# Kernel optimization log

Hardware: AMD Instinct MI355X
Metric: run time of the kernel (lower is better)

Reference implementation:

```python
import jax, jax.numpy as jnp
import numpy as np

B, LS, VS = 4, 1024, 1024
VH, LH, H = 1024, 1024, 16
HD = LH // H  # head_dim = 64


def setup_inputs() -> dict:
    key = jax.random.key(0)
    ks = jax.random.split(key, 10)
    s = 0.02
    return {
        "v_hidden_states": jax.random.normal(ks[0], (B, VS, VH), jnp.float32),
        "l_hidden_states": jax.random.normal(ks[1], (B, LS, LH), jnp.float32),
        "q_w": jax.random.normal(ks[2], (LH, LH), jnp.float32) * s,
        "q_b": jnp.zeros((LH,), jnp.float32),
        "k_w": jax.random.normal(ks[3], (VH, LH), jnp.float32) * s,
        "k_b": jnp.zeros((LH,), jnp.float32),
        "v_w": jax.random.normal(ks[4], (VH, LH), jnp.float32) * s,
        "v_b": jnp.zeros((LH,), jnp.float32),
        "o_w": jax.random.normal(ks[5], (LH, LH), jnp.float32) * s,
        "o_b": jnp.zeros((LH,), jnp.float32),
    }


def reference(v_hidden_states, l_hidden_states, q_w, q_b, k_w, k_b, v_w, v_b, o_w, o_b):
    b, ls, _ = l_hidden_states.shape
    vs = v_hidden_states.shape[1]
    q = (l_hidden_states @ q_w + q_b).reshape(b, ls, H, HD)
    k = (v_hidden_states @ k_w + k_b).reshape(b, vs, H, HD)
    v = (v_hidden_states @ v_w + v_b).reshape(b, vs, H, HD)
    # NOTE: original scales by sqrt(hidden_size), not sqrt(head_dim)
    scale = jnp.sqrt(jnp.asarray(LH, q.dtype))
    scores = jnp.einsum("blhd,bvhd->bhlv", q, k) / scale
    attn = jax.nn.softmax(scores, axis=-1)
    out = jnp.einsum("bhlv,bvhd->blhd", attn, v).reshape(b, ls, LH)
    return out @ o_w + o_b
```

## Files before the change

kernel.cpp:

```cpp
#include <hip/hip_runtime.h>

typedef __bf16 bf16;
typedef __attribute__((ext_vector_type(4))) __bf16 bf16x4;
typedef __attribute__((ext_vector_type(8))) __bf16 bf16x8;
typedef __attribute__((ext_vector_type(4))) float f32x4;

static __device__ __forceinline__ f32x4 mfma_16x16x32(bf16x8 a, bf16x8 b, f32x4 c) {
    return __builtin_amdgcn_mfma_f32_16x16x32_bf16(a, b, c, 0, 0, 0);
}

static __device__ __forceinline__ bf16x8 load8(const float* p) {
    f32x4 a = *(const f32x4*)p;
    f32x4 b = *(const f32x4*)(p + 4);
    bf16x8 r;
    r[0] = (bf16)a[0]; r[1] = (bf16)a[1]; r[2] = (bf16)a[2]; r[3] = (bf16)a[3];
    r[4] = (bf16)b[0]; r[5] = (bf16)b[1]; r[6] = (bf16)b[2]; r[7] = (bf16)b[3];
    return r;
}

static __device__ __forceinline__ void gload_lds16(const void* g, void* l) {
    __builtin_amdgcn_global_load_lds(
        (const __attribute__((address_space(1))) void*)g,
        (__attribute__((address_space(3))) void*)l, 16, 0, 0);
}

__global__ __launch_bounds__(256) void prep_kernel(
    const float* __restrict__ l_h, const float* __restrict__ v_h,
    const float* __restrict__ w0, const float* __restrict__ w1,
    const float* __restrict__ w2, const float* __restrict__ w3,
    bf16* __restrict__ l_bf, bf16* __restrict__ v_bf,
    bf16* __restrict__ dq, bf16* __restrict__ dkv, bf16* __restrict__ dov)
{
    const int id = blockIdx.x;
    if (id < 4096) {
        const float* s = (id < 2048) ? l_h : v_h;
        bf16*       d = (id < 2048) ? l_bf : v_bf;
        const int   bb = (id < 2048) ? id : id - 2048;
        const size_t i = ((size_t)bb * 256 + threadIdx.x) * 8;
        *(bf16x8*)(d + i) = load8(s + i);
        return;
    }
    const int widx = id - 4096;
    const int z    = widx >> 8;
    const int rem  = widx & 255;
    const int j0   = (rem & 15) * 64;
    const int i0   = (rem >> 4) * 64;
    const float* src; bf16* dst;
    switch (z) {
        case 0:  src = w0; dst = dq; break;
        case 1:  src = w1; dst = dkv; break;
        case 2:  src = w2; dst = dkv + (size_t)1024 * 1024; break;
        default: src = w3; dst = dov; break;
    }
    __shared__ float T[64][65];
    const int tx = threadIdx.x & 15;
    const int ty = threadIdx.x >> 4;
    #pragma unroll
    for (int it = 0; it < 4; ++it) {
        f32x4 v = *(const f32x4*)(src + (size_t)(i0 + ty + it * 16) * 1024 + j0 + tx * 4);
        T[ty + it * 16][tx * 4 + 0] = v[0];
        T[ty + it * 16][tx * 4 + 1] = v[1];
        T[ty + it * 16][tx * 4 + 2] = v[2];
        T[ty + it * 16][tx * 4 + 3] = v[3];
    }
    __syncthreads();
    #pragma unroll
    for (int it = 0; it < 4; ++it) {
        const int jj = ty + it * 16;
        bf16x4 o;
        o[0] = (bf16)T[tx * 4 + 0][jj];
        o[1] = (bf16)T[tx * 4 + 1][jj];
        o[2] = (bf16)T[tx * 4 + 2][jj];
        o[3] = (bf16)T[tx * 4 + 3][jj];
        *(bf16x4*)(dst + (size_t)(j0 + jj) * 1024 + i0 + tx * 4) = o;
    }
}

__global__ __launch_bounds__(256, 2) void proj128_kernel(
    const bf16* __restrict__ l_bf, const bf16* __restrict__ v_bf,
    const bf16* __restrict__ QWt,  const bf16* __restrict__ KVWt,
    const float* __restrict__ q_b, const float* __restrict__ k_b,
    const float* __restrict__ v_b,
    bf16* __restrict__ Qh, bf16* __restrict__ Kh, bf16* __restrict__ Vt)
{
    __shared__ __align__(16) bf16 As[128][32];
    __shared__ __align__(16) bf16 Bs[128][32];

    const int t    = threadIdx.x;
    const int lane = t & 63;
    const int wave = t >> 6;
    const int wm   = wave & 1;
    const int wn   = wave >> 1;
    const int l15  = lane & 15;
    const int quad = lane >> 4;

    const bool isQ = blockIdx.x < 8;
    const bf16* A  = isQ ? l_bf : v_bf;
    const bf16* Bt = isQ ? QWt  : KVWt;
    const int  gn0 = (isQ ? blockIdx.x : blockIdx.x - 8) * 128;
    const int  gm0 = blockIdx.y * 128;
    const int  K   = 1024;

    const int srow    = lane >> 2;
    const int chunk_g = (lane & 3) ^ ((srow >> 1) & 3);
    const size_t aoff = (size_t)(gm0 + wave * 32 + srow) * K + chunk_g * 8;
    const size_t boff = (size_t)(gn0 + wave * 32 + srow) * K + chunk_g * 8;

    f32x4 acc[4][4];
    #pragma unroll
    for (int i = 0; i < 4; ++i)
        #pragma unroll
        for (int j = 0; j < 4; ++j)
            acc[i][j] = (f32x4){0.f, 0.f, 0.f, 0.f};

    for (int k0 = 0; k0 < K; k0 += 32) {
        #pragma unroll
        for (int q = 0; q < 2; ++q) {
            gload_lds16(A  + aoff + (size_t)q * 16 * K + k0, &As[wave * 32 + q * 16][0]);
            gload_lds16(Bt + boff + (size_t)q * 16 * K + k0, &Bs[wave * 32 + q * 16][0]);
        }
        __syncthreads();

        bf16x8 af[4], bfr[4];
        #pragma unroll
        for (int mt = 0; mt < 4; ++mt) {
            const int row = wm * 64 + mt * 16 + l15;
            af[mt] = *(const bf16x8*)(&As[row][(quad ^ ((row >> 1) & 3)) * 8]);
        }
        #pragma unroll
        for (int nt = 0; nt < 4; ++nt) {
            const int row = wn * 64 + nt * 16 + l15;
            bfr[nt] = *(const bf16x8*)(&Bs[row][(quad ^ ((row >> 1) & 3)) * 8]);
        }
        #pragma unroll
        for (int mt = 0; mt < 4; ++mt)
            #pragma unroll
            for (int nt = 0; nt < 4; ++nt)
                acc[mt][nt] = mfma_16x16x32(af[mt], bfr[nt], acc[mt][nt]);

        __syncthreads();
    }

    #pragma unroll
    for (int nt = 0; nt < 4; ++nt) {
        const int col = gn0 + wn * 64 + nt * 16 + l15;
        float bb; bf16* dst; bool hm;
        if (isQ)             { bb = q_b[col];        dst = Qh; hm = true;  }
        else if (col < 1024) { bb = k_b[col];        dst = Kh; hm = true;  }
        else                 { bb = v_b[col - 1024]; dst = Vt; hm = false; }
        #pragma unroll
        for (int mt = 0; mt < 4; ++mt) {
            #pragma unroll
            for (int r = 0; r < 4; ++r) {
                const int row = gm0 + wm * 64 + mt * 16 + quad * 4 + r;
                const float v = acc[mt][nt][r] + bb;
                if (hm) {
                    const size_t idx =
                        ((size_t)((row >> 10) * 16 + (col >> 6)) * 1024 +
                         (row & 1023)) * 64 + (col & 63);
                    dst[idx] = (bf16)v;
                } else {
                    const int vc = col - 1024;
                    const size_t idx =
                        ((size_t)((row >> 10) * 16 + (vc >> 6)) * 64 +
                         (vc & 63)) * 1024 + (row & 1023);
                    dst[idx] = (bf16)v;
                }
            }
        }
    }
}

static __device__ __forceinline__ void gemm_core_128x64(
    const bf16* __restrict__ A, const bf16* __restrict__ Bt, int K,
    int gm0, int gn0, bf16 (*As)[32], bf16 (*Bs)[32], f32x4 acc[4][2])
{
    const int t    = threadIdx.x;
    const int lane = t & 63;
    const int wave = t >> 6;
    const int wm   = wave & 1;
    const int wn   = wave >> 1;
    const int l15  = lane & 15;
    const int quad = lane >> 4;

    const int srow    = lane >> 2;
    const int chunk_g = (lane & 3) ^ ((srow >> 1) & 3);
    const size_t aoff = (size_t)(gm0 + wave * 32 + srow) * K + chunk_g * 8;
    const size_t boff = (size_t)(gn0 + wave * 16 + srow) * K + chunk_g * 8;

    #pragma unroll
    for (int i = 0; i < 4; ++i)
        #pragma unroll
        for (int j = 0; j < 2; ++j)
            acc[i][j] = (f32x4){0.f, 0.f, 0.f, 0.f};

    for (int k0 = 0; k0 < K; k0 += 32) {
        gload_lds16(A + aoff + k0,                  &As[wave * 32][0]);
        gload_lds16(A + aoff + (size_t)16 * K + k0, &As[wave * 32 + 16][0]);
        gload_lds16(Bt + boff + k0,                 &Bs[wave * 16][0]);
        __syncthreads();

        bf16x8 af[4], bfr[2];
        #pragma unroll
        for (int mt = 0; mt < 4; ++mt) {
            const int row = wm * 64 + mt * 16 + l15;
            af[mt] = *(const bf16x8*)(&As[row][(quad ^ ((row >> 1) & 3)) * 8]);
        }
        #pragma unroll
        for (int nt = 0; nt < 2; ++nt) {
            const int row = wn * 32 + nt * 16 + l15;
            bfr[nt] = *(const bf16x8*)(&Bs[row][(quad ^ ((row >> 1) & 3)) * 8]);
        }
        #pragma unroll
        for (int mt = 0; mt < 4; ++mt)
            #pragma unroll
            for (int nt = 0; nt < 2; ++nt)
                acc[mt][nt] = mfma_16x16x32(af[mt], bfr[nt], acc[mt][nt]);

        __syncthreads();
    }
}

__global__ __launch_bounds__(256, 3) void ogemm_kernel(
    const bf16* __restrict__ Aw, const bf16* __restrict__ OWt,
    const float* __restrict__ o_b, float* __restrict__ C)
{
    __shared__ __align__(16) bf16 As[128][32];
    __shared__ __align__(16) bf16 Bs[64][32];

    const int gn0 = blockIdx.x * 64;
    const int gm0 = blockIdx.y * 128;

    f32x4 acc[4][2];
    gemm_core_128x64(Aw, OWt, 1024, gm0, gn0, As, Bs, acc);

    const int lane = threadIdx.x & 63;
    const int wave = threadIdx.x >> 6;
    const int wm   = wave & 1;
    const int wn   = wave >> 1;
    const int l15  = lane & 15;
    const int quad = lane >> 4;

    #pragma unroll
    for (int nt = 0; nt < 2; ++nt) {
        const int col = gn0 + wn * 32 + nt * 16 + l15;
        const float bb = o_b[col];
        #pragma unroll
        for (int mt = 0; mt < 4; ++mt) {
            #pragma unroll
            for (int r = 0; r < 4; ++r) {
                const int row = gm0 + wm * 64 + mt * 16 + quad * 4 + r;
                C[(size_t)row * 1024 + col] = acc[mt][nt][r] + bb;
            }
        }
    }
}

__global__ __launch_bounds__(256) void attn_kernel(
    const bf16* __restrict__ Q, const bf16* __restrict__ K,
    const bf16* __restrict__ V, bf16* __restrict__ O)
{
    const int t    = threadIdx.x;
    const int lane = t & 63;
    const int wave = t >> 6;
    const int l15  = lane & 15;
    const int quad = lane >> 4;
    const int qg   = wave & 1;
    const int kvh  = wave >> 1;

    const int head = blockIdx.x;
    const int q0   = blockIdx.y * 64;
    const int b    = head >> 4;
    const int h    = head & 15;

    __shared__ __align__(16) bf16 P[4][32][72];
    __shared__ float combO[2][32][64];
    __shared__ float combL[2][8][64];

    const bf16* Qp  = Q + ((size_t)head * 1024 + q0 + qg * 32) * 64;
    const bf16* Kp  = K + (size_t)head * 1024 * 64;
    const bf16* Vtp = V + (size_t)head * 64 * 1024;

    bf16x8 aq[2][2];
    #pragma unroll
    for (int mt = 0; mt < 2; ++mt)
        #pragma unroll
        for (int kc = 0; kc < 2; ++kc)
            aq[mt][kc] = *(const bf16x8*)(Qp + (mt * 16 + l15) * 64 + kc * 32 + quad * 8);

    f32x4 oacc[2][4];
    #pragma unroll
    for (int mt = 0; mt < 2; ++mt)
        #pragma unroll
        for (int nt = 0; nt < 4; ++nt)
            oacc[mt][nt] = (f32x4){0.f, 0.f, 0.f, 0.f};
    float lsum[2][4];
    #pragma unroll
    for (int mt = 0; mt < 2; ++mt)
        #pragma unroll
        for (int r = 0; r < 4; ++r) lsum[mt][r] = 0.f;

    const float scale = 0.03125f;

    for (int c = 0; c < 8; ++c) {
        const int kv0 = kvh * 512 + c * 64;

        bf16x8 bk[4][2];
        #pragma unroll
        for (int nt = 0; nt < 4; ++nt) {
            const bf16* kp = Kp + (size_t)(kv0 + nt * 16 + l15) * 64 + quad * 8;
            bk[nt][0] = *(const bf16x8*)(kp);
            bk[nt][1] = *(const bf16x8*)(kp + 32);
        }
        bf16x8 bv[4][2];
        #pragma unroll
        for (int nt = 0; nt < 4; ++nt) {
            const bf16* vp = Vtp + (size_t)(nt * 16 + l15) * 1024 + kv0 + quad * 8;
            bv[nt][0] = *(const bf16x8*)(vp);
            bv[nt][1] = *(const bf16x8*)(vp + 32);
        }

        #pragma unroll
        for (int mt = 0; mt < 2; ++mt) {
            #pragma unroll
            for (int nt = 0; nt < 4; ++nt) {
                f32x4 s = (f32x4){0.f, 0.f, 0.f, 0.f};
                s = mfma_16x16x32(aq[mt][0], bk[nt][0], s);
                s = mfma_16x16x32(aq[mt][1], bk[nt][1], s);
                #pragma unroll
                for (int r = 0; r < 4; ++r) {
                    const float e = __expf(s[r] * scale);
                    lsum[mt][r] += e;
                    P[wave][mt * 16 + quad * 4 + r][nt * 16 + l15] = (bf16)e;
                }
            }
        }

        #pragma unroll
        for (int mt = 0; mt < 2; ++mt) {
            bf16x8 pa0 = *(const bf16x8*)(&P[wave][mt * 16 + l15][quad * 8]);
            bf16x8 pa1 = *(const bf16x8*)(&P[wave][mt * 16 + l15][32 + quad * 8]);
            #pragma unroll
            for (int nt = 0; nt < 4; ++nt) {
                oacc[mt][nt] = mfma_16x16x32(pa0, bv[nt][0], oacc[mt][nt]);
                oacc[mt][nt] = mfma_16x16x32(pa1, bv[nt][1], oacc[mt][nt]);
            }
        }
    }

    if (kvh == 1) {
        #pragma unroll
        for (int mt = 0; mt < 2; ++mt) {
            #pragma unroll
            for (int nt = 0; nt < 4; ++nt)
                #pragma unroll
                for (int r = 0; r < 4; ++r)
                    combO[qg][mt * 16 + nt * 4 + r][lane] = oacc[mt][nt][r];
            #pragma unroll
            for (int r = 0; r < 4; ++r)
                combL[qg][mt * 4 + r][lane] = lsum[mt][r];
        }
    }
    __syncthreads();
    if (kvh == 0) {
        #pragma unroll
        for (int mt = 0; mt < 2; ++mt) {
            #pragma unroll
            for (int nt = 0; nt < 4; ++nt)
                #pragma unroll
                for (int r = 0; r < 4; ++r)
                    oacc[mt][nt][r] += combO[qg][mt * 16 + nt * 4 + r][lane];
            #pragma unroll
            for (int r = 0; r < 4; ++r)
                lsum[mt][r] += combL[qg][mt * 4 + r][lane];
        }

        #pragma unroll
        for (int off = 1; off <= 8; off <<= 1)
            #pragma unroll
            for (int mt = 0; mt < 2; ++mt)
                #pragma unroll
                for (int r = 0; r < 4; ++r)
                    lsum[mt][r] += __shfl_xor(lsum[mt][r], off, 64);

        #pragma unroll
        for (int mt = 0; mt < 2; ++mt) {
            const float invs[4] = {1.0f / lsum[mt][0], 1.0f / lsum[mt][1],
                                   1.0f / lsum[mt][2], 1.0f / lsum[mt][3]};
            #pragma unroll
            for (int nt = 0; nt < 4; ++nt) {
                #pragma unroll
                for (int r = 0; r < 4; ++r) {
                    const int row = q0 + qg * 32 + mt * 16 + quad * 4 + r;
                    O[((size_t)b * 1024 + row) * 1024 + h * 64 + nt * 16 + l15] =
                        (bf16)(oacc[mt][nt][r] * invs[r]);
                }
            }
        }
    }
}

extern "C" void kernel_launch(void* const* d_in, const int* in_sizes, int n_in,
                              void* d_out, int out_size, void* d_ws, size_t ws_size,
                              hipStream_t stream)
{
    const float* v_h = (const float*)d_in[0];
    const float* l_h = (const float*)d_in[1];
    const float* q_w = (const float*)d_in[2];
    const float* q_b = (const float*)d_in[3];
    const float* k_w = (const float*)d_in[4];
    const float* k_b = (const float*)d_in[5];
    const float* v_w = (const float*)d_in[6];
    const float* v_b = (const float*)d_in[7];
    const float* o_w = (const float*)d_in[8];
    const float* o_b = (const float*)d_in[9];
    float* out = (float*)d_out;

    const size_t SZ = (size_t)4096 * 1024;
    const size_t WZ = (size_t)1024 * 1024;

    bf16* l_bf = (bf16*)d_ws;
    bf16* v_bf = l_bf + SZ;
    bf16* QWt  = v_bf + SZ;
    bf16* KVWt = QWt + WZ;
    bf16* OWt  = KVWt + 2 * WZ;
    bf16* Qh   = OWt + WZ;
    bf16* Kh   = Qh + SZ;
    bf16* Vt   = Kh + SZ;
    bf16* Aw   = Vt + SZ;

    prep_kernel<<<dim3(5120), 256, 0, stream>>>(
        l_h, v_h, q_w, k_w, v_w, o_w, l_bf, v_bf, QWt, KVWt, OWt);

    proj128_kernel<<<dim3(24, 32), 256, 0, stream>>>(
        l_bf, v_bf, QWt, KVWt, q_b, k_b, v_b, Qh, Kh, Vt);

    attn_kernel<<<dim3(64, 16), 256, 0, stream>>>(Qh, Kh, Vt, Aw);

    ogemm_kernel<<<dim3(16, 32), 256, 0, stream>>>(Aw, OWt, o_b, out);

    (void)in_sizes; (void)n_in; (void)out_size; (void)ws_size;
}
```

Measured before the change: 226.4 us.

## Stage K/V through double-buffered LDS in attention and fold softmax scale into Q weights

```diff
diff --git a/kernel.cpp b/kernel.cpp
--- a/kernel.cpp
+++ b/kernel.cpp
@@ -52,6 +52,7 @@
         case 2:  src = w2; dst = dkv + (size_t)1024 * 1024; break;
         default: src = w3; dst = dov; break;
     }
+    const float wscale = (z == 0) ? 0.03125f : 1.0f;
     __shared__ float T[64][65];
     const int tx = threadIdx.x & 15;
     const int ty = threadIdx.x >> 4;
@@ -68,10 +69,10 @@
     for (int it = 0; it < 4; ++it) {
         const int jj = ty + it * 16;
         bf16x4 o;
-        o[0] = (bf16)T[tx * 4 + 0][jj];
-        o[1] = (bf16)T[tx * 4 + 1][jj];
-        o[2] = (bf16)T[tx * 4 + 2][jj];
-        o[3] = (bf16)T[tx * 4 + 3][jj];
+        o[0] = (bf16)(T[tx * 4 + 0][jj] * wscale);
+        o[1] = (bf16)(T[tx * 4 + 1][jj] * wscale);
+        o[2] = (bf16)(T[tx * 4 + 2][jj] * wscale);
+        o[3] = (bf16)(T[tx * 4 + 3][jj] * wscale);
         *(bf16x4*)(dst + (size_t)(j0 + jj) * 1024 + i0 + tx * 4) = o;
     }
 }
@@ -145,9 +146,9 @@
     for (int nt = 0; nt < 4; ++nt) {
         const int col = gn0 + wn * 64 + nt * 16 + l15;
         float bb; bf16* dst; bool hm;
-        if (isQ)             { bb = q_b[col];        dst = Qh; hm = true;  }
-        else if (col < 1024) { bb = k_b[col];        dst = Kh; hm = true;  }
-        else                 { bb = v_b[col - 1024]; dst = Vt; hm = false; }
+        if (isQ)             { bb = q_b[col] * 0.03125f; dst = Qh; hm = true;  }
+        else if (col < 1024) { bb = k_b[col];            dst = Kh; hm = true;  }
+        else                 { bb = v_b[col - 1024];     dst = Vt; hm = false; }
         #pragma unroll
         for (int mt = 0; mt < 4; ++mt) {
             #pragma unroll
@@ -265,21 +266,23 @@
     const int wave = t >> 6;
     const int l15  = lane & 15;
     const int quad = lane >> 4;
-    const int qg   = wave & 1;
-    const int kvh  = wave >> 1;
 
     const int head = blockIdx.x;
-    const int q0   = blockIdx.y * 64;
+    const int q0   = blockIdx.y * 128;
     const int b    = head >> 4;
     const int h    = head & 15;
 
+    __shared__ __align__(16) bf16 Kb[2][64][64];
+    __shared__ __align__(16) bf16 Vb[2][64][64];
     __shared__ __align__(16) bf16 P[4][32][72];
-    __shared__ float combO[2][32][64];
-    __shared__ float combL[2][8][64];
-
-    const bf16* Qp  = Q + ((size_t)head * 1024 + q0 + qg * 32) * 64;
+
+    const bf16* Qp  = Q + ((size_t)head * 1024 + q0 + wave * 32) * 64;
     const bf16* Kp  = K + (size_t)head * 1024 * 64;
     const bf16* Vtp = V + (size_t)head * 64 * 1024;
+
+    const int r8  = lane >> 3;
+    const int c8  = lane & 7;
+    const int swz = (c8 ^ r8) * 8;
 
     bf16x8 aq[2][2];
     #pragma unroll
@@ -300,36 +303,41 @@
         #pragma unroll
         for (int r = 0; r < 4; ++r) lsum[mt][r] = 0.f;
 
-    const float scale = 0.03125f;
-
-    for (int c = 0; c < 8; ++c) {
-        const int kv0 = kvh * 512 + c * 64;
-
-        bf16x8 bk[4][2];
+    #define STAGE(c, buf)                                                          \
+        {                                                                          \
+            const int kv0_ = (c) * 64;                                             \
+            _Pragma("unroll")                                                      \
+            for (int g = 0; g < 2; ++g) {                                          \
+                const int R = wave * 16 + g * 8;                                   \
+                gload_lds16(Kp + (size_t)(kv0_ + R + r8) * 64 + swz,               \
+                            &Kb[buf][R][0]);                                       \
+                gload_lds16(Vtp + (size_t)(R + r8) * 1024 + kv0_ + swz,            \
+                            &Vb[buf][R][0]);                                       \
+            }                                                                      \
+        }
+
+    STAGE(0, 0);
+
+    const int sw = l15 & 7;
+
+    for (int c = 0; c < 16; ++c) {
+        const int buf = c & 1;
+        __syncthreads();
+        if (c + 1 < 16) STAGE(c + 1, buf ^ 1);
+
         #pragma unroll
         for (int nt = 0; nt < 4; ++nt) {
-            const bf16* kp = Kp + (size_t)(kv0 + nt * 16 + l15) * 64 + quad * 8;
-            bk[nt][0] = *(const bf16x8*)(kp);
-            bk[nt][1] = *(const bf16x8*)(kp + 32);
-        }
-        bf16x8 bv[4][2];
-        #pragma unroll
-        for (int nt = 0; nt < 4; ++nt) {
-            const bf16* vp = Vtp + (size_t)(nt * 16 + l15) * 1024 + kv0 + quad * 8;
-            bv[nt][0] = *(const bf16x8*)(vp);
-            bv[nt][1] = *(const bf16x8*)(vp + 32);
-        }
-
-        #pragma unroll
-        for (int mt = 0; mt < 2; ++mt) {
-            #pragma unroll
-            for (int nt = 0; nt < 4; ++nt) {
+            const bf16* krow = &Kb[buf][nt * 16 + l15][0];
+            bf16x8 bk0 = *(const bf16x8*)(krow + (quad ^ sw) * 8);
+            bf16x8 bk1 = *(const bf16x8*)(krow + ((quad + 4) ^ sw) * 8);
+            #pragma unroll
+            for (int mt = 0; mt < 2; ++mt) {
                 f32x4 s = (f32x4){0.f, 0.f, 0.f, 0.f};
-                s = mfma_16x16x32(aq[mt][0], bk[nt][0], s);
-                s = mfma_16x16x32(aq[mt][1], bk[nt][1], s);
+                s = mfma_16x16x32(aq[mt][0], bk0, s);
+                s = mfma_16x16x32(aq[mt][1], bk1, s);
                 #pragma unroll
                 for (int r = 0; r < 4; ++r) {
-                    const float e = __expf(s[r] * scale);
+                    const float e = __expf(s[r]);
                     lsum[mt][r] += e;
                     P[wave][mt * 16 + quad * 4 + r][nt * 16 + l15] = (bf16)e;
                 }
@@ -342,59 +350,35 @@
             bf16x8 pa1 = *(const bf16x8*)(&P[wave][mt * 16 + l15][32 + quad * 8]);
             #pragma unroll
             for (int nt = 0; nt < 4; ++nt) {
-                oacc[mt][nt] = mfma_16x16x32(pa0, bv[nt][0], oacc[mt][nt]);
-                oacc[mt][nt] = mfma_16x16x32(pa1, bv[nt][1], oacc[mt][nt]);
+                const bf16* vrow = &Vb[buf][nt * 16 + l15][0];
+                bf16x8 bv0 = *(const bf16x8*)(vrow + (quad ^ sw) * 8);
+                bf16x8 bv1 = *(const bf16x8*)(vrow + ((quad + 4) ^ sw) * 8);
+                oacc[mt][nt] = mfma_16x16x32(pa0, bv0, oacc[mt][nt]);
+                oacc[mt][nt] = mfma_16x16x32(pa1, bv1, oacc[mt][nt]);
             }
         }
     }
-
-    if (kvh == 1) {
-        #pragma unroll
-        for (int mt = 0; mt < 2; ++mt) {
-            #pragma unroll
-            for (int nt = 0; nt < 4; ++nt)
-                #pragma unroll
-                for (int r = 0; r < 4; ++r)
-                    combO[qg][mt * 16 + nt * 4 + r][lane] = oacc[mt][nt][r];
+    #undef STAGE
+
+    #pragma unroll
+    for (int off = 1; off <= 8; off <<= 1)
+        #pragma unroll
+        for (int mt = 0; mt < 2; ++mt)
             #pragma unroll
             for (int r = 0; r < 4; ++r)
-                combL[qg][mt * 4 + r][lane] = lsum[mt][r];
-        }
-    }
-    __syncthreads();
-    if (kvh == 0) {
-        #pragma unroll
-        for (int mt = 0; mt < 2; ++mt) {
-            #pragma unroll
-            for (int nt = 0; nt < 4; ++nt)
-                #pragma unroll
-                for (int r = 0; r < 4; ++r)
-                    oacc[mt][nt][r] += combO[qg][mt * 16 + nt * 4 + r][lane];
-            #pragma unroll
-            for (int r = 0; r < 4; ++r)
-                lsum[mt][r] += combL[qg][mt * 4 + r][lane];
-        }
-
-        #pragma unroll
-        for (int off = 1; off <= 8; off <<= 1)
-            #pragma unroll
-            for (int mt = 0; mt < 2; ++mt)
-                #pragma unroll
-                for (int r = 0; r < 4; ++r)
-                    lsum[mt][r] += __shfl_xor(lsum[mt][r], off, 64);
-
-        #pragma unroll
-        for (int mt = 0; mt < 2; ++mt) {
-            const float invs[4] = {1.0f / lsum[mt][0], 1.0f / lsum[mt][1],
-                                   1.0f / lsum[mt][2], 1.0f / lsum[mt][3]};
-            #pragma unroll
-            for (int nt = 0; nt < 4; ++nt) {
-                #pragma unroll
-                for (int r = 0; r < 4; ++r) {
-                    const int row = q0 + qg * 32 + mt * 16 + quad * 4 + r;
-                    O[((size_t)b * 1024 + row) * 1024 + h * 64 + nt * 16 + l15] =
-                        (bf16)(oacc[mt][nt][r] * invs[r]);
-                }
+                lsum[mt][r] += __shfl_xor(lsum[mt][r], off, 64);
+
+    #pragma unroll
+    for (int mt = 0; mt < 2; ++mt) {
+        const float invs[4] = {1.0f / lsum[mt][0], 1.0f / lsum[mt][1],
+                               1.0f / lsum[mt][2], 1.0f / lsum[mt][3]};
+        #pragma unroll
+        for (int nt = 0; nt < 4; ++nt) {
+            #pragma unroll
+            for (int r = 0; r < 4; ++r) {
+                const int row = q0 + wave * 32 + mt * 16 + quad * 4 + r;
+                O[((size_t)b * 1024 + row) * 1024 + h * 64 + nt * 16 + l15] =
+                    (bf16)(oacc[mt][nt][r] * invs[r]);
             }
         }
     }
@@ -435,7 +419,7 @@
     proj128_kernel<<<dim3(24, 32), 256, 0, stream>>>(
         l_bf, v_bf, QWt, KVWt, q_b, k_b, v_b, Qh, Kh, Vt);
 
-    attn_kernel<<<dim3(64, 16), 256, 0, stream>>>(Qh, Kh, Vt, Aw);
+    attn_kernel<<<dim3(64, 8), 256, 0, stream>>>(Qh, Kh, Vt, Aw);
 
     ogemm_kernel<<<dim3(16, 32), 256, 0, stream>>>(Aw, OWt, o_b, out);
 
```

New measurement: 195.5 us. 1.16x faster.
